# Performance work log

Hardware: AMD Instinct MI355X
Metric: run time of the kernel (lower is better)

Reference implementation:

```python
import jax, jax.numpy as jnp
import numpy as np

N, E, R, D = 50000, 800000, 8, 64
BN_EPS = 1e-5


def _bn_relu(x, g, b):
    # training-mode BatchNorm1d (biased variance) + relu
    m = x.mean(axis=0)
    v = x.var(axis=0)
    return jax.nn.relu((x - m) / jnp.sqrt(v + BN_EPS) * g + b)


def setup_inputs() -> dict:
    key = jax.random.key(0)
    ks = jax.random.split(key, 10)
    return {
        'x': jax.random.normal(ks[0], (N, D), dtype=jnp.float32),
        'edge_weight': jax.random.uniform(ks[1], (E,), dtype=jnp.float32),
        'W_lin1': jax.random.normal(ks[2], (D, R * D), dtype=jnp.float32) * 0.05,
        'b_lin1': jnp.zeros((D,), jnp.float32),
        'W_self1': jax.random.normal(ks[3], (D, D), dtype=jnp.float32) * 0.05,
        'b_self1': jnp.zeros((D,), jnp.float32),
        'gamma1': jnp.ones((D,), jnp.float32),
        'beta1': jnp.zeros((D,), jnp.float32),
        'W_lin2': jax.random.normal(ks[4], (D, D), dtype=jnp.float32) * 0.05,
        'b_lin2': jnp.zeros((D,), jnp.float32),
        'W_self2': jax.random.normal(ks[5], (D, D), dtype=jnp.float32) * 0.05,
        'b_self2': jnp.zeros((D,), jnp.float32),
        'gamma2': jnp.ones((D,), jnp.float32),
        'beta2': jnp.zeros((D,), jnp.float32),
        'node_in': jax.random.randint(ks[6], (E,), 0, N, dtype=jnp.int32),
        'node_out': jax.random.randint(ks[7], (E,), 0, N, dtype=jnp.int32),
        'relation': jax.random.randint(ks[8], (E,), 0, R, dtype=jnp.int32),
        'num_relation': R,
    }


def reference(x, edge_weight, W_lin1, b_lin1, W_self1, b_self1, gamma1, beta1,
              W_lin2, b_lin2, W_self2, b_self2, gamma2, beta2,
              node_in, node_out, relation, num_relation):
    Nn, Din = x.shape
    Rr = int(num_relation)
    seg = node_out * Rr + relation  # node_out * num_relation + relation
    # degree normalization of edge weights (shared by both layers)
    deg = jax.ops.segment_sum(edge_weight, seg, num_segments=Nn * Rr)
    ew = edge_weight / deg[seg]

    # layer 1: relationalGraphConv
    msgs = x[node_in] * ew[:, None]  # [E, D]
    upd = jax.ops.segment_sum(msgs, seg, num_segments=Nn * Rr)
    upd = upd.reshape(Nn, Rr * Din)  # node-major flatten, matches torch .view
    h = upd @ W_lin1.T + b_lin1 + x @ W_self1.T + b_self1
    h = _bn_relu(h, gamma1, beta1)  # [N, D]

    # layer 2: relationalGraph (per-relation outputs)
    msgs2 = h[node_in] * ew[:, None]
    upd2 = jax.ops.segment_sum(msgs2, seg, num_segments=Nn * Rr)  # [N*R, D] node-major
    upd2 = upd2.reshape(Nn, Rr, -1).transpose(1, 0, 2).reshape(Rr * Nn, -1)  # relation-major
    h_rep = jnp.tile(h, (Rr, 1))  # input.repeat(R, 1)
    out = upd2 @ W_lin2.T + b_lin2 + h_rep @ W_self2.T + b_self2
    out = _bn_relu(out, gamma2, beta2)
    return out.reshape(Rr, Nn, -1)
```

## Files before the change

### kernel.cpp

```cpp
#include <hip/hip_runtime.h>


#define GATHER_GRID 2048
#define SCAN_CHUNK 4096
#define RED_BLOCKS 64
#define ZERO_BLOCKS 256
#define PACK_BLOCKS 16
#define COUNT_BLOCKS 2048
#define PLACE_BLOCKS 1024

typedef short bf16x8 __attribute__((ext_vector_type(8)));
typedef float f32x4 __attribute__((ext_vector_type(4)));

static __device__ __forceinline__ float bf2f(unsigned short u) {
  return __uint_as_float(((unsigned)u) << 16);
}
static __device__ __forceinline__ unsigned short f2bf(float f) {
  unsigned u = __float_as_uint(f);
  u += 0x7FFFu + ((u >> 16) & 1u);
  return (unsigned short)(u >> 16);
}

__global__ void k_zeropack(int* __restrict__ cnt, int NR, int R,
                           const float* __restrict__ Wlin1, const float* __restrict__ Wself1,
                           const float* __restrict__ Wlin2, const float* __restrict__ Wself2,
                           unsigned short* __restrict__ wb1, unsigned short* __restrict__ wb2) {
  if (blockIdx.x < ZERO_BLOCKS) {
    int i = blockIdx.x * 256 + threadIdx.x;
    int stride = ZERO_BLOCKS * 256;
    for (int k = i; k < NR; k += stride) cnt[k] = 0;
  } else {
    int i = (blockIdx.x - ZERO_BLOCKS) * 256 + threadIdx.x;
    int stride = PACK_BLOCKS * 256;
    int n1 = (R + 1) * 64 * 64;
    int n2 = 2 * 64 * 64;
    for (int k = i; k < n1 + n2; k += stride) {
      if (k < n1) {
        int r = k >> 6, d = k & 63;
        float v;
        if (r < R * 64) {
          int s = r >> 6, j = r & 63;
          v = Wlin1[j * (R * 64) + s * 64 + d];
        } else {
          v = Wself1[(r - R * 64) * 64 + d];
        }
        wb1[k] = f2bf(v);
      } else {
        int k2 = k - n1;
        int r = k2 >> 6, d = k2 & 63;
        float v = (r < 64) ? Wlin2[r * 64 + d] : Wself2[(r - 64) * 64 + d];
        wb2[k2] = f2bf(v);
      }
    }
  }
}

__global__ __launch_bounds__(256) void k_countgemm(
    const int* __restrict__ node_out, const int* __restrict__ rel,
    int* __restrict__ cnt, int* __restrict__ tmp, int E, int R,
    const float* __restrict__ xf, int M, const unsigned short* __restrict__ Wb,
    unsigned short* __restrict__ outLinB, unsigned short* __restrict__ outSelf,
    int mblocks) {
  if ((int)blockIdx.x < mblocks) {
    int m0 = blockIdx.x * 64;
    int wid = threadIdx.x >> 6;
    int lane = threadIdx.x & 63;
    int mrow = m0 + wid * 16 + (lane & 15);
    int mload = (mrow < M) ? mrow : (M - 1);
    const float* arow = xf + (size_t)mload * 64 + 8 * (lane >> 4);
    float4 af0 = *(const float4*)(arow);
    float4 af1 = *(const float4*)(arow + 4);
    float4 af2 = *(const float4*)(arow + 32);
    float4 af3 = *(const float4*)(arow + 36);
    bf16x8 a0, a1;
    a0[0] = (short)f2bf(af0.x); a0[1] = (short)f2bf(af0.y);
    a0[2] = (short)f2bf(af0.z); a0[3] = (short)f2bf(af0.w);
    a0[4] = (short)f2bf(af1.x); a0[5] = (short)f2bf(af1.y);
    a0[6] = (short)f2bf(af1.z); a0[7] = (short)f2bf(af1.w);
    a1[0] = (short)f2bf(af2.x); a1[1] = (short)f2bf(af2.y);
    a1[2] = (short)f2bf(af2.z); a1[3] = (short)f2bf(af2.w);
    a1[4] = (short)f2bf(af3.x); a1[5] = (short)f2bf(af3.y);
    a1[6] = (short)f2bf(af3.z); a1[7] = (short)f2bf(af3.w);
    int rbase = m0 + wid * 16 + ((lane >> 4) << 2);
    int cbase = lane & 15;
    for (int slab = 0; slab <= R; ++slab) {
      const unsigned short* wrow = Wb + ((size_t)slab * 64 + (lane & 15)) * 64 + 8 * (lane >> 4);
      unsigned short* op = (slab < R) ? (outLinB + (size_t)slab * M * 64) : outSelf;
      #pragma unroll
      for (int nt = 0; nt < 4; ++nt) {
        bf16x8 b0 = *(const bf16x8*)(wrow + nt * 16 * 64);
        bf16x8 b1 = *(const bf16x8*)(wrow + nt * 16 * 64 + 32);
        f32x4 c = {};
        c = __builtin_amdgcn_mfma_f32_16x16x32_bf16(a0, b0, c, 0, 0, 0);
        c = __builtin_amdgcn_mfma_f32_16x16x32_bf16(a1, b1, c, 0, 0, 0);
        int col = nt * 16 + cbase;
        #pragma unroll
        for (int rg = 0; rg < 4; ++rg) {
          int grow = rbase + rg;
          if (grow < M) op[(size_t)grow * 64 + col] = f2bf(c[rg]);
        }
      }
    }
  } else {
    int i = ((int)blockIdx.x - mblocks) * 256 + threadIdx.x;
    int stride = COUNT_BLOCKS * 256;
    for (int e = i; e < E; e += stride) {
      int seg = node_out[e] * R + rel[e];
      tmp[e] = atomicAdd(&cnt[seg], 1);
    }
  }
}

__global__ __launch_bounds__(256) void k_scan1(const int* __restrict__ cnt,
                                               int* __restrict__ bsum, int NR) {
  __shared__ int red[256];
  int tid = threadIdx.x;
  int base = blockIdx.x * SCAN_CHUNK;
  int s = 0;
  for (int i = tid; i < SCAN_CHUNK; i += 256) {
    int idx = base + i;
    if (idx < NR) s += cnt[idx];
  }
  red[tid] = s;
  __syncthreads();
  for (int off = 128; off > 0; off >>= 1) {
    if (tid < off) red[tid] += red[tid + off];
    __syncthreads();
  }
  if (tid == 0) bsum[blockIdx.x] = red[0];
}

__global__ void k_scan2(const int* __restrict__ bsum, int* __restrict__ bpre,
                        int* __restrict__ rowptr_end, int NB) {
  int lane = threadIdx.x;
  int carry = 0;
  for (int base = 0; base < NB; base += 64) {
    int i = base + lane;
    int v = (i < NB) ? bsum[i] : 0;
    int incl = v;
    #pragma unroll
    for (int off = 1; off < 64; off <<= 1) {
      int u = __shfl_up(incl, off);
      if (lane >= off) incl += u;
    }
    if (i < NB) bpre[i] = carry + incl - v;
    carry += __shfl(incl, 63);
  }
  if (lane == 0) *rowptr_end = carry;
}

__global__ __launch_bounds__(256) void k_scan3(const int* __restrict__ cnt,
                                               const int* __restrict__ bpre,
                                               int* __restrict__ rowptr,
                                               unsigned* __restrict__ descT,
                                               int NR, int R, int Nn) {
  __shared__ int wtot[4];
  int tid = threadIdx.x, lane = tid & 63, wid = tid >> 6;
  int base = blockIdx.x * SCAN_CHUNK + tid * 16;
  int v[16];
  int t = 0;
  #pragma unroll
  for (int i = 0; i < 16; i++) {
    int idx = base + i;
    v[i] = (idx < NR) ? cnt[idx] : 0;
    t += v[i];
  }
  int incl = t;
  #pragma unroll
  for (int off = 1; off < 64; off <<= 1) {
    int u = __shfl_up(incl, off);
    if (lane >= off) incl += u;
  }
  if (lane == 63) wtot[wid] = incl;
  __syncthreads();
  int woff = 0;
  for (int w = 0; w < wid; w++) woff += wtot[w];
  int start = bpre[blockIdx.x] + woff + incl - t;
  #pragma unroll
  for (int i = 0; i < 16; i++) {
    int idx = base + i;
    if (idx < NR) {
      rowptr[idx] = start;
      int n = (int)((unsigned)idx / (unsigned)R);
      int r = idx - n * R;
      descT[(size_t)r * Nn + n] = (unsigned)start | ((unsigned)v[i] << 20);
    }
    start += v[i];
  }
}

__global__ void k_place(const float* __restrict__ w, const int* __restrict__ node_out,
                        const int* __restrict__ node_in, const int* __restrict__ rel,
                        const int* __restrict__ rowptr, const int* __restrict__ tmp,
                        unsigned* __restrict__ ep4, int E, int R) {
  int i = blockIdx.x * blockDim.x + threadIdx.x;
  int stride = gridDim.x * blockDim.x;
  for (int e = i; e < E; e += stride) {
    int seg = node_out[e] * R + rel[e];
    int pos = rowptr[seg] + tmp[e];
    ep4[pos] = (unsigned)node_in[e] | ((unsigned)f2bf(w[e]) << 16);
  }
}

__global__ __launch_bounds__(256) void k_gather1(
    const int* __restrict__ rowptr, const unsigned* __restrict__ ep4,
    const unsigned short* __restrict__ y1, const unsigned short* __restrict__ s1,
    unsigned short* __restrict__ h_pre, float* __restrict__ part, int N, int R) {
  int lane = threadIdx.x & 63;
  int wid = threadIdx.x >> 6;
  int l16 = lane & 15;
  int lg = lane >> 4;
  int c0 = l16 * 4;
  int grp = blockIdx.x * 16 + wid * 4 + lg;
  int ngrp = gridDim.x * 16;
  float lsum[4] = {0.f, 0.f, 0.f, 0.f}, lsq[4] = {0.f, 0.f, 0.f, 0.f};
  for (int n = grp; n < N; n += ngrp) {
    int segbase = n * R;
    int k = rowptr[segbase];
    float t0 = 0.f, t1 = 0.f, t2 = 0.f, t3 = 0.f;
    for (int r = 0; r < R; r++) {
      int k1 = rowptr[segbase + r + 1];
      if (k < k1) {
        const unsigned short* yb = y1 + (size_t)r * N * 64;
        float a0 = 0.f, a1 = 0.f, a2 = 0.f, a3 = 0.f, d = 0.f;
        for (; k + 1 < k1; k += 2) {
          unsigned pA = ep4[k], pB = ep4[k + 1];
          ushort4 uA = *(const ushort4*)&yb[(size_t)(pA & 0xFFFFu) * 64 + c0];
          ushort4 uB = *(const ushort4*)&yb[(size_t)(pB & 0xFFFFu) * 64 + c0];
          float wA = bf2f((unsigned short)(pA >> 16));
          float wB = bf2f((unsigned short)(pB >> 16));
          d += wA + wB;
          a0 = fmaf(wA, bf2f(uA.x), a0); a1 = fmaf(wA, bf2f(uA.y), a1);
          a2 = fmaf(wA, bf2f(uA.z), a2); a3 = fmaf(wA, bf2f(uA.w), a3);
          a0 = fmaf(wB, bf2f(uB.x), a0); a1 = fmaf(wB, bf2f(uB.y), a1);
          a2 = fmaf(wB, bf2f(uB.z), a2); a3 = fmaf(wB, bf2f(uB.w), a3);
        }
        if (k < k1) {
          unsigned p = ep4[k];
          float w = bf2f((unsigned short)(p >> 16));
          ushort4 u = *(const ushort4*)&yb[(size_t)(p & 0xFFFFu) * 64 + c0];
          d += w;
          a0 = fmaf(w, bf2f(u.x), a0); a1 = fmaf(w, bf2f(u.y), a1);
          a2 = fmaf(w, bf2f(u.z), a2); a3 = fmaf(w, bf2f(u.w), a3);
        }
        if (d != 0.f) {
          float inv = 1.f / d;
          t0 = fmaf(a0, inv, t0); t1 = fmaf(a1, inv, t1);
          t2 = fmaf(a2, inv, t2); t3 = fmaf(a3, inv, t3);
        }
        k = k1;
      }
    }
    ushort4 su = *(const ushort4*)&s1[(size_t)n * 64 + c0];
    float v0 = t0 + bf2f(su.x), v1 = t1 + bf2f(su.y);
    float v2 = t2 + bf2f(su.z), v3 = t3 + bf2f(su.w);
    ushort4 o; o.x = f2bf(v0); o.y = f2bf(v1); o.z = f2bf(v2); o.w = f2bf(v3);
    *(ushort4*)&h_pre[(size_t)n * 64 + c0] = o;
    lsum[0] += v0; lsq[0] += v0 * v0;
    lsum[1] += v1; lsq[1] += v1 * v1;
    lsum[2] += v2; lsq[2] += v2 * v2;
    lsum[3] += v3; lsq[3] += v3 * v3;
  }
  __shared__ float sp[16][64], sq[16][64];
  int g = wid * 4 + lg;
  #pragma unroll
  for (int i = 0; i < 4; i++) { sp[g][c0 + i] = lsum[i]; sq[g][c0 + i] = lsq[i]; }
  __syncthreads();
  if (threadIdx.x < 64) {
    int j = threadIdx.x;
    float s = 0.f, q = 0.f;
    #pragma unroll
    for (int gg = 0; gg < 16; gg++) { s += sp[gg][j]; q += sq[gg][j]; }
    part[(size_t)blockIdx.x * 128 + j] = s;
    part[(size_t)blockIdx.x * 128 + 64 + j] = q;
  }
}

__global__ __launch_bounds__(256) void k_gemm2bn(
    const unsigned short* __restrict__ hp, int M,
    const unsigned short* __restrict__ Wb, int nslab,
    const float* __restrict__ ss,
    unsigned short* __restrict__ outLinB, unsigned short* __restrict__ outSelf) {
  __shared__ float sss[128];
  if (threadIdx.x < 128) sss[threadIdx.x] = ss[threadIdx.x];
  __syncthreads();
  int m0 = blockIdx.x * 64;
  int wid = threadIdx.x >> 6;
  int lane = threadIdx.x & 63;
  int mrow = m0 + wid * 16 + (lane & 15);
  int mload = (mrow < M) ? mrow : (M - 1);
  int cb = 8 * (lane >> 4);
  const unsigned short* arow = hp + (size_t)mload * 64 + cb;
  ushort4 u0 = *(const ushort4*)(arow);
  ushort4 u1 = *(const ushort4*)(arow + 4);
  ushort4 u2 = *(const ushort4*)(arow + 32);
  ushort4 u3 = *(const ushort4*)(arow + 36);
  bf16x8 a0, a1;
  #pragma unroll
  for (int j = 0; j < 4; j++) {
    unsigned short uu0 = (&u0.x)[j], uu1 = (&u1.x)[j], uu2 = (&u2.x)[j], uu3 = (&u3.x)[j];
    a0[j]     = (short)f2bf(fmaxf(fmaf(bf2f(uu0), sss[cb + j],      sss[64 + cb + j]), 0.f));
    a0[j + 4] = (short)f2bf(fmaxf(fmaf(bf2f(uu1), sss[cb + 4 + j],  sss[64 + cb + 4 + j]), 0.f));
    a1[j]     = (short)f2bf(fmaxf(fmaf(bf2f(uu2), sss[cb + 32 + j], sss[64 + cb + 32 + j]), 0.f));
    a1[j + 4] = (short)f2bf(fmaxf(fmaf(bf2f(uu3), sss[cb + 36 + j], sss[64 + cb + 36 + j]), 0.f));
  }
  int rbase = m0 + wid * 16 + ((lane >> 4) << 2);
  int cbase = lane & 15;
  for (int slab = 0; slab <= nslab; ++slab) {
    const unsigned short* wrow = Wb + ((size_t)slab * 64 + (lane & 15)) * 64 + 8 * (lane >> 4);
    unsigned short* op = (slab < nslab) ? (outLinB + (size_t)slab * M * 64) : outSelf;
    #pragma unroll
    for (int nt = 0; nt < 4; ++nt) {
      bf16x8 b0 = *(const bf16x8*)(wrow + nt * 16 * 64);
      bf16x8 b1 = *(const bf16x8*)(wrow + nt * 16 * 64 + 32);
      f32x4 c = {};
      c = __builtin_amdgcn_mfma_f32_16x16x32_bf16(a0, b0, c, 0, 0, 0);
      c = __builtin_amdgcn_mfma_f32_16x16x32_bf16(a1, b1, c, 0, 0, 0);
      int col = nt * 16 + cbase;
      #pragma unroll
      for (int rg = 0; rg < 4; ++rg) {
        int grow = rbase + rg;
        if (grow < M) op[(size_t)grow * 64 + col] = f2bf(c[rg]);
      }
    }
  }
}

__global__ __launch_bounds__(256) void k_gather2_stats(
    const unsigned* __restrict__ descT, const unsigned* __restrict__ ep4,
    const unsigned short* __restrict__ z, const unsigned short* __restrict__ s2,
    float* __restrict__ part, int N, int R) {
  int lane = threadIdx.x & 63;
  int wid = threadIdx.x >> 6;
  int l16 = lane & 15;
  int lg = lane >> 4;
  int c0 = l16 * 4;
  int grp = blockIdx.x * 16 + wid * 4 + lg;
  int ngrp = gridDim.x * 16;
  int NR = N * R;
  float lsum[4] = {0.f, 0.f, 0.f, 0.f}, lsq[4] = {0.f, 0.f, 0.f, 0.f};
  for (int s = grp; s < NR; s += ngrp) {
    unsigned r = (unsigned)s / (unsigned)N;
    int n = s - (int)r * N;
    unsigned desc = descT[s];
    int k = (int)(desc & 0xFFFFFu);
    int cnt = (int)(desc >> 20);
    int k1 = k + cnt;
    float a0 = 0.f, a1 = 0.f, a2 = 0.f, a3 = 0.f, d = 0.f;
    for (; k + 1 < k1; k += 2) {
      unsigned pA = ep4[k], pB = ep4[k + 1];
      ushort4 uA = *(const ushort4*)&z[(size_t)(pA & 0xFFFFu) * 64 + c0];
      ushort4 uB = *(const ushort4*)&z[(size_t)(pB & 0xFFFFu) * 64 + c0];
      float wA = bf2f((unsigned short)(pA >> 16));
      float wB = bf2f((unsigned short)(pB >> 16));
      d += wA + wB;
      a0 = fmaf(wA, bf2f(uA.x), a0); a1 = fmaf(wA, bf2f(uA.y), a1);
      a2 = fmaf(wA, bf2f(uA.z), a2); a3 = fmaf(wA, bf2f(uA.w), a3);
      a0 = fmaf(wB, bf2f(uB.x), a0); a1 = fmaf(wB, bf2f(uB.y), a1);
      a2 = fmaf(wB, bf2f(uB.z), a2); a3 = fmaf(wB, bf2f(uB.w), a3);
    }
    if (k < k1) {
      unsigned p = ep4[k];
      float w = bf2f((unsigned short)(p >> 16));
      ushort4 u = *(const ushort4*)&z[(size_t)(p & 0xFFFFu) * 64 + c0];
      d += w;
      a0 = fmaf(w, bf2f(u.x), a0); a1 = fmaf(w, bf2f(u.y), a1);
      a2 = fmaf(w, bf2f(u.z), a2); a3 = fmaf(w, bf2f(u.w), a3);
    }
    if (d != 0.f) {
      float inv = 1.f / d;
      a0 *= inv; a1 *= inv; a2 *= inv; a3 *= inv;
    }
    ushort4 su = *(const ushort4*)&s2[(size_t)n * 64 + c0];
    float v0 = a0 + bf2f(su.x), v1 = a1 + bf2f(su.y);
    float v2 = a2 + bf2f(su.z), v3 = a3 + bf2f(su.w);
    lsum[0] += v0; lsq[0] += v0 * v0;
    lsum[1] += v1; lsq[1] += v1 * v1;
    lsum[2] += v2; lsq[2] += v2 * v2;
    lsum[3] += v3; lsq[3] += v3 * v3;
  }
  __shared__ float sp[16][64], sq[16][64];
  int g = wid * 4 + lg;
  #pragma unroll
  for (int i = 0; i < 4; i++) { sp[g][c0 + i] = lsum[i]; sq[g][c0 + i] = lsq[i]; }
  __syncthreads();
  if (threadIdx.x < 64) {
    int j = threadIdx.x;
    float s = 0.f, q = 0.f;
    #pragma unroll
    for (int gg = 0; gg < 16; gg++) { s += sp[gg][j]; q += sq[gg][j]; }
    part[(size_t)blockIdx.x * 128 + j] = s;
    part[(size_t)blockIdx.x * 128 + 64 + j] = q;
  }
}

__global__ __launch_bounds__(256) void k_gather2_write(
    const unsigned* __restrict__ descT, const unsigned* __restrict__ ep4,
    const unsigned short* __restrict__ z, const unsigned short* __restrict__ s2,
    const float* __restrict__ ss, float* __restrict__ out, int N, int R) {
  int lane = threadIdx.x & 63;
  int wid = threadIdx.x >> 6;
  int l16 = lane & 15;
  int lg = lane >> 4;
  int c0 = l16 * 4;
  float sc0 = ss[c0], sc1 = ss[c0 + 1], sc2 = ss[c0 + 2], sc3 = ss[c0 + 3];
  float sh0 = ss[64 + c0], sh1 = ss[64 + c0 + 1], sh2 = ss[64 + c0 + 2], sh3 = ss[64 + c0 + 3];
  int grp = blockIdx.x * 16 + wid * 4 + lg;
  int ngrp = gridDim.x * 16;
  int NR = N * R;
  for (int s = grp; s < NR; s += ngrp) {
    unsigned r = (unsigned)s / (unsigned)N;
    int n = s - (int)r * N;
    unsigned desc = descT[s];
    int k = (int)(desc & 0xFFFFFu);
    int cnt = (int)(desc >> 20);
    int k1 = k + cnt;
    float a0 = 0.f, a1 = 0.f, a2 = 0.f, a3 = 0.f, d = 0.f;
    for (; k + 1 < k1; k += 2) {
      unsigned pA = ep4[k], pB = ep4[k + 1];
      ushort4 uA = *(const ushort4*)&z[(size_t)(pA & 0xFFFFu) * 64 + c0];
      ushort4 uB = *(const ushort4*)&z[(size_t)(pB & 0xFFFFu) * 64 + c0];
      float wA = bf2f((unsigned short)(pA >> 16));
      float wB = bf2f((unsigned short)(pB >> 16));
      d += wA + wB;
      a0 = fmaf(wA, bf2f(uA.x), a0); a1 = fmaf(wA, bf2f(uA.y), a1);
      a2 = fmaf(wA, bf2f(uA.z), a2); a3 = fmaf(wA, bf2f(uA.w), a3);
      a0 = fmaf(wB, bf2f(uB.x), a0); a1 = fmaf(wB, bf2f(uB.y), a1);
      a2 = fmaf(wB, bf2f(uB.z), a2); a3 = fmaf(wB, bf2f(uB.w), a3);
    }
    if (k < k1) {
      unsigned p = ep4[k];
      float w = bf2f((unsigned short)(p >> 16));
      ushort4 u = *(const ushort4*)&z[(size_t)(p & 0xFFFFu) * 64 + c0];
      d += w;
      a0 = fmaf(w, bf2f(u.x), a0); a1 = fmaf(w, bf2f(u.y), a1);
      a2 = fmaf(w, bf2f(u.z), a2); a3 = fmaf(w, bf2f(u.w), a3);
    }
    if (d != 0.f) {
      float inv = 1.f / d;
      a0 *= inv; a1 *= inv; a2 *= inv; a3 *= inv;
    }
    ushort4 su = *(const ushort4*)&s2[(size_t)n * 64 + c0];
    float v0 = fmaxf(fmaf(a0 + bf2f(su.x), sc0, sh0), 0.f);
    float v1 = fmaxf(fmaf(a1 + bf2f(su.y), sc1, sh1), 0.f);
    float v2 = fmaxf(fmaf(a2 + bf2f(su.z), sc2, sh2), 0.f);
    float v3 = fmaxf(fmaf(a3 + bf2f(su.w), sc3, sh3), 0.f);
    *(float4*)&out[(size_t)s * 64 + c0] = make_float4(v0, v1, v2, v3);
  }
}

__global__ __launch_bounds__(256) void k_red1(const float* __restrict__ part,
                                              float* __restrict__ part2, int P) {
  int j = threadIdx.x & 127;
  int g = threadIdx.x >> 7;
  int rows = (P + RED_BLOCKS - 1) / RED_BLOCKS;
  int base = blockIdx.x * rows;
  float acc = 0.f;
  for (int i = g; i < rows; i += 2) {
    int idx = base + i;
    if (idx < P) acc += part[(size_t)idx * 128 + j];
  }
  __shared__ float red[2][128];
  red[g][j] = acc;
  __syncthreads();
  if (threadIdx.x < 128) part2[(size_t)blockIdx.x * 128 + j] = red[0][j] + red[1][j];
}

__global__ __launch_bounds__(1024) void k_bnstats(
    const float* __restrict__ part, int P, float M,
    const float* __restrict__ gamma, const float* __restrict__ beta,
    float* __restrict__ ss) {
  __shared__ float red[1024];
  int tid = threadIdx.x;
  int j = tid & 127;
  int g = tid >> 7;
  float acc = 0.f;
  for (int i = g; i < P; i += 8) acc += part[(size_t)i * 128 + j];
  red[tid] = acc;
  __syncthreads();
  if (tid < 128) {
    float s = 0.f;
    for (int gg = 0; gg < 8; gg++) s += red[gg * 128 + tid];
    red[tid] = s;
  }
  __syncthreads();
  if (tid < 64) {
    float s = red[tid], q = red[64 + tid];
    float mean = s / M;
    float var = q / M - mean * mean;
    float sc = gamma[tid] / sqrtf(var + 1e-5f);
    ss[tid] = sc;
    ss[64 + tid] = beta[tid] - mean * sc;
  }
}

extern "C" void kernel_launch(void* const* d_in, const int* in_sizes, int n_in,
                              void* d_out, int out_size, void* d_ws, size_t ws_size,
                              hipStream_t stream) {
  const float* x        = (const float*)d_in[0];
  const float* edge_w   = (const float*)d_in[1];
  const float* W_lin1   = (const float*)d_in[2];
  const float* W_self1  = (const float*)d_in[4];
  const float* gamma1   = (const float*)d_in[6];
  const float* beta1    = (const float*)d_in[7];
  const float* W_lin2   = (const float*)d_in[8];
  const float* W_self2  = (const float*)d_in[10];
  const float* gamma2   = (const float*)d_in[12];
  const float* beta2    = (const float*)d_in[13];
  const int* node_in    = (const int*)d_in[14];
  const int* node_out   = (const int*)d_in[15];
  const int* relation   = (const int*)d_in[16];

  int N = in_sizes[0] / 64;
  int E = in_sizes[1];
  int R = in_sizes[2] / (64 * 64);
  int NR = N * R;
  int NB = (NR + SCAN_CHUNK - 1) / SCAN_CHUNK;

  char* p = (char*)d_ws;
  auto alloc = [&](size_t bytes) { char* r = p; p += (bytes + 255) & ~(size_t)255; return r; };
  int* cnt      = (int*)alloc(4ull * NR);
  int* rowptr   = (int*)alloc(4ull * (NR + 1));
  unsigned* descT = (unsigned*)alloc(4ull * NR);
  int* tmp      = (int*)alloc(4ull * E);
  int* bsum     = (int*)alloc(4ull * NB);
  int* bpre     = (int*)alloc(4ull * NB);
  unsigned* ep4 = (unsigned*)alloc(4ull * E);
  unsigned short* wb1 = (unsigned short*)alloc(2ull * (R + 1) * 64 * 64);
  unsigned short* wb2 = (unsigned short*)alloc(2ull * 2 * 64 * 64);
  unsigned short* s1    = (unsigned short*)alloc(2ull * N * 64);
  unsigned short* h_pre = (unsigned short*)alloc(2ull * N * 64);
  unsigned short* z     = (unsigned short*)alloc(2ull * N * 64);
  unsigned short* s2    = (unsigned short*)alloc(2ull * N * 64);
  float* part   = (float*)alloc(4ull * GATHER_GRID * 128);
  float* part2  = (float*)alloc(4ull * RED_BLOCKS * 128);
  float* ss1    = (float*)alloc(4ull * 128);
  float* ss2    = (float*)alloc(4ull * 128);

  unsigned short* y1 = (unsigned short*)d_out;

  int mblocks = (N + 63) / 64;

  k_zeropack<<<ZERO_BLOCKS + PACK_BLOCKS, 256, 0, stream>>>(
      cnt, NR, R, W_lin1, W_self1, W_lin2, W_self2, wb1, wb2);
  k_countgemm<<<mblocks + COUNT_BLOCKS, 256, 0, stream>>>(
      node_out, relation, cnt, tmp, E, R, x, N, wb1, y1, s1, mblocks);
  k_scan1<<<NB, 256, 0, stream>>>(cnt, bsum, NR);
  k_scan2<<<1, 64, 0, stream>>>(bsum, bpre, &rowptr[NR], NB);
  k_scan3<<<NB, 256, 0, stream>>>(cnt, bpre, rowptr, descT, NR, R, N);
  k_place<<<PLACE_BLOCKS, 256, 0, stream>>>(
      edge_w, node_out, node_in, relation, rowptr, tmp, ep4, E, R);

  k_gather1<<<GATHER_GRID, 256, 0, stream>>>(rowptr, ep4, y1, s1, h_pre, part, N, R);
  k_red1<<<RED_BLOCKS, 256, 0, stream>>>(part, part2, GATHER_GRID);
  k_bnstats<<<1, 1024, 0, stream>>>(part2, RED_BLOCKS, (float)N, gamma1, beta1, ss1);

  k_gemm2bn<<<mblocks, 256, 0, stream>>>(h_pre, N, wb2, 1, ss1, z, s2);
  k_gather2_stats<<<GATHER_GRID, 256, 0, stream>>>(descT, ep4, z, s2, part, N, R);
  k_red1<<<RED_BLOCKS, 256, 0, stream>>>(part, part2, GATHER_GRID);
  k_bnstats<<<1, 1024, 0, stream>>>(part2, RED_BLOCKS, (float)N * R, gamma2, beta2, ss2);
  k_gather2_write<<<GATHER_GRID, 256, 0, stream>>>(descT, ep4, z, s2, ss2, (float*)d_out, N, R);
}
```

Measured before the change: 256.1 us.

## Stash layer-2 pre-activations in output buffer instead of re-gathering for BN

The layer-2 stats pass now also writes bf16 pre-activations into the first half of each output row in d_out. A new elementwise in-place kernel then applies the BN scale/shift and ReLU, replacing the second full edge gather. This removes a second pass of random neighbor loads at the cost of an extra 6.4MB bf16 write plus a read back. It also adds bf16 rounding of the pre-activation and relies on each row's bf16 slot (bytes 0-127) being read before its float slot (bytes 0-255) overwrites it, which holds within one thread.

```diff
diff --git a/kernel.cpp b/kernel.cpp
--- a/kernel.cpp
+++ b/kernel.cpp
@@ -326,10 +326,10 @@
   }
 }
 
-__global__ __launch_bounds__(256) void k_gather2_stats(
+__global__ __launch_bounds__(256) void k_gather2_statsave(
     const unsigned* __restrict__ descT, const unsigned* __restrict__ ep4,
     const unsigned short* __restrict__ z, const unsigned short* __restrict__ s2,
-    float* __restrict__ part, int N, int R) {
+    float* __restrict__ part, unsigned short* __restrict__ pre, int N, int R) {
   int lane = threadIdx.x & 63;
   int wid = threadIdx.x >> 6;
   int l16 = lane & 15;
@@ -374,6 +374,8 @@
     ushort4 su = *(const ushort4*)&s2[(size_t)n * 64 + c0];
     float v0 = a0 + bf2f(su.x), v1 = a1 + bf2f(su.y);
     float v2 = a2 + bf2f(su.z), v3 = a3 + bf2f(su.w);
+    ushort4 o; o.x = f2bf(v0); o.y = f2bf(v1); o.z = f2bf(v2); o.w = f2bf(v3);
+    *(ushort4*)&pre[(size_t)s * 128 + c0] = o;
     lsum[0] += v0; lsq[0] += v0 * v0;
     lsum[1] += v1; lsq[1] += v1 * v1;
     lsum[2] += v2; lsq[2] += v2 * v2;
@@ -394,57 +396,24 @@
   }
 }
 
-__global__ __launch_bounds__(256) void k_gather2_write(
-    const unsigned* __restrict__ descT, const unsigned* __restrict__ ep4,
-    const unsigned short* __restrict__ z, const unsigned short* __restrict__ s2,
-    const float* __restrict__ ss, float* __restrict__ out, int N, int R) {
-  int lane = threadIdx.x & 63;
-  int wid = threadIdx.x >> 6;
-  int l16 = lane & 15;
-  int lg = lane >> 4;
+__global__ __launch_bounds__(256) void k_bnrelu_inplace(
+    float* __restrict__ out, const float* __restrict__ ss, int NR) {
+  __shared__ float sss[128];
+  if (threadIdx.x < 128) sss[threadIdx.x] = ss[threadIdx.x];
+  __syncthreads();
+  int l16 = threadIdx.x & 15;
   int c0 = l16 * 4;
-  float sc0 = ss[c0], sc1 = ss[c0 + 1], sc2 = ss[c0 + 2], sc3 = ss[c0 + 3];
-  float sh0 = ss[64 + c0], sh1 = ss[64 + c0 + 1], sh2 = ss[64 + c0 + 2], sh3 = ss[64 + c0 + 3];
-  int grp = blockIdx.x * 16 + wid * 4 + lg;
-  int ngrp = gridDim.x * 16;
-  int NR = N * R;
-  for (int s = grp; s < NR; s += ngrp) {
-    unsigned r = (unsigned)s / (unsigned)N;
-    int n = s - (int)r * N;
-    unsigned desc = descT[s];
-    int k = (int)(desc & 0xFFFFFu);
-    int cnt = (int)(desc >> 20);
-    int k1 = k + cnt;
-    float a0 = 0.f, a1 = 0.f, a2 = 0.f, a3 = 0.f, d = 0.f;
-    for (; k + 1 < k1; k += 2) {
-      unsigned pA = ep4[k], pB = ep4[k + 1];
-      ushort4 uA = *(const ushort4*)&z[(size_t)(pA & 0xFFFFu) * 64 + c0];
-      ushort4 uB = *(const ushort4*)&z[(size_t)(pB & 0xFFFFu) * 64 + c0];
-      float wA = bf2f((unsigned short)(pA >> 16));
-      float wB = bf2f((unsigned short)(pB >> 16));
-      d += wA + wB;
-      a0 = fmaf(wA, bf2f(uA.x), a0); a1 = fmaf(wA, bf2f(uA.y), a1);
-      a2 = fmaf(wA, bf2f(uA.z), a2); a3 = fmaf(wA, bf2f(uA.w), a3);
-      a0 = fmaf(wB, bf2f(uB.x), a0); a1 = fmaf(wB, bf2f(uB.y), a1);
-      a2 = fmaf(wB, bf2f(uB.z), a2); a3 = fmaf(wB, bf2f(uB.w), a3);
-    }
-    if (k < k1) {
-      unsigned p = ep4[k];
-      float w = bf2f((unsigned short)(p >> 16));
-      ushort4 u = *(const ushort4*)&z[(size_t)(p & 0xFFFFu) * 64 + c0];
-      d += w;
-      a0 = fmaf(w, bf2f(u.x), a0); a1 = fmaf(w, bf2f(u.y), a1);
-      a2 = fmaf(w, bf2f(u.z), a2); a3 = fmaf(w, bf2f(u.w), a3);
-    }
-    if (d != 0.f) {
-      float inv = 1.f / d;
-      a0 *= inv; a1 *= inv; a2 *= inv; a3 *= inv;
-    }
-    ushort4 su = *(const ushort4*)&s2[(size_t)n * 64 + c0];
-    float v0 = fmaxf(fmaf(a0 + bf2f(su.x), sc0, sh0), 0.f);
-    float v1 = fmaxf(fmaf(a1 + bf2f(su.y), sc1, sh1), 0.f);
-    float v2 = fmaxf(fmaf(a2 + bf2f(su.z), sc2, sh2), 0.f);
-    float v3 = fmaxf(fmaf(a3 + bf2f(su.w), sc3, sh3), 0.f);
+  float sc0 = sss[c0], sc1 = sss[c0 + 1], sc2 = sss[c0 + 2], sc3 = sss[c0 + 3];
+  float sh0 = sss[64 + c0], sh1 = sss[64 + c0 + 1], sh2 = sss[64 + c0 + 2], sh3 = sss[64 + c0 + 3];
+  int row = blockIdx.x * 16 + (threadIdx.x >> 4);
+  int stride = gridDim.x * 16;
+  const unsigned short* pre = (const unsigned short*)out;
+  for (int s = row; s < NR; s += stride) {
+    ushort4 u = *(const ushort4*)&pre[(size_t)s * 128 + c0];
+    float v0 = fmaxf(fmaf(bf2f(u.x), sc0, sh0), 0.f);
+    float v1 = fmaxf(fmaf(bf2f(u.y), sc1, sh1), 0.f);
+    float v2 = fmaxf(fmaf(bf2f(u.z), sc2, sh2), 0.f);
+    float v3 = fmaxf(fmaf(bf2f(u.w), sc3, sh3), 0.f);
     *(float4*)&out[(size_t)s * 64 + c0] = make_float4(v0, v1, v2, v3);
   }
 }
@@ -556,8 +525,9 @@
   k_bnstats<<<1, 1024, 0, stream>>>(part2, RED_BLOCKS, (float)N, gamma1, beta1, ss1);
 
   k_gemm2bn<<<mblocks, 256, 0, stream>>>(h_pre, N, wb2, 1, ss1, z, s2);
-  k_gather2_stats<<<GATHER_GRID, 256, 0, stream>>>(descT, ep4, z, s2, part, N, R);
+  k_gather2_statsave<<<GATHER_GRID, 256, 0, stream>>>(
+      descT, ep4, z, s2, part, (unsigned short*)d_out, N, R);
   k_red1<<<RED_BLOCKS, 256, 0, stream>>>(part, part2, GATHER_GRID);
   k_bnstats<<<1, 1024, 0, stream>>>(part2, RED_BLOCKS, (float)N * R, gamma2, beta2, ss2);
-  k_gather2_write<<<GATHER_GRID, 256, 0, stream>>>(descT, ep4, z, s2, ss2, (float*)d_out, N, R);
-}
+  k_bnrelu_inplace<<<4096, 256, 0, stream>>>((float*)d_out, ss2, NR);
+}
```

Measured after the change: 239.4 us. -6.5%, faster.
